# Kernel optimization log

Measured on AMD Instinct MI355X. Metric: run time of the kernel, lower is better.

## Reference

```python
import jax, jax.numpy as jnp
import numpy as np

STATE_SIZE, ACTION_SIZE, REWARD_SIZE = 128, 16, 4
IN = STATE_SIZE + REWARD_SIZE  # 132
B = 8192
W_NUM = 32


def _linear_params(key, fin, fout):
    k1, k2 = jax.random.split(key)
    s = 1.0 / np.sqrt(fin)
    w = jax.random.uniform(k1, (fout, fin), jnp.float32, -s, s)
    b = jax.random.uniform(k2, (fout,), jnp.float32, -s, s)
    return w, b


def setup_inputs() -> dict:
    key = jax.random.key(0)
    ks = jax.random.split(key, 7)
    w1, b1 = _linear_params(ks[0], IN, IN * 16)        # 132 -> 2112
    w2, b2 = _linear_params(ks[1], IN * 16, IN * 32)   # 2112 -> 4224
    w3, b3 = _linear_params(ks[2], IN * 32, IN * 64)   # 4224 -> 8448
    w4, b4 = _linear_params(ks[3], IN * 64, IN * 32)   # 8448 -> 4224
    wq, bq = _linear_params(ks[4], IN * 32, ACTION_SIZE * REWARD_SIZE)
    state = jax.random.normal(ks[5], (B, STATE_SIZE), jnp.float32)
    preference = jax.random.uniform(ks[6], (B, REWARD_SIZE), jnp.float32)
    return dict(state=state, preference=preference,
                w1=w1, b1=b1, w2=w2, b2=b2, w3=w3, b3=b3, w4=w4, b4=b4,
                wq=wq, bq=bq, w_num=W_NUM)


def _forward(state, preference, w1, b1, w2, b2, w3, b3, w4, b4, wq, bq, w_num):
    x = jnp.concatenate([state, preference], axis=1)              # [B, IN]
    h = jax.nn.relu(x @ w1.T + b1)
    h = jax.nn.relu(h @ w2.T + b2)
    h = jax.nn.relu(h @ w3.T + b3)
    h = jax.nn.relu(h @ w4.T + b4)
    q = (h @ wq.T + bq).reshape(-1, ACTION_SIZE, REWARD_SIZE)     # [B, A, R]

    s_num = preference.shape[0] // w_num
    # H(): envelope operator. The torch code repeat_interleaves flat_Q w_num
    # times per group; within each (w, s) group the preference vector is
    # constant, so inner products are constant across each run of w_num
    # repeated rows. argmax(dim=1)//w_num therefore equals argmax over the
    # action axis (first-tie semantics match). We compute that directly
    # without the O(w_num^2) blow-up -- identical math, identical output.
    qd = jax.lax.stop_gradient(q)                                 # Q.detach()
    rq = qd.reshape(s_num, w_num, ACTION_SIZE, REWARD_SIZE)
    rq = jnp.transpose(rq, (1, 0, 2, 3))                          # [w, s, A, R]
    rw = jnp.transpose(preference.reshape(s_num, w_num, REWARD_SIZE), (1, 0, 2))  # [w, s, R]
    ip = jnp.einsum('wsar,wsr->wsa', rq, rw)                      # [w, s, A]
    a_star = jnp.argmax(ip, axis=2)                               # [w, s]
    hq = jnp.take_along_axis(rq, a_star[..., None, None], axis=2)[:, :, 0, :]  # [w, s, R]
    hq = jnp.transpose(hq, (1, 0, 2)).reshape(-1, REWARD_SIZE)    # [s*w, R]
    return hq, q


def reference(state, preference, w1, b1, w2, b2, w3, b3, w4, b4, wq, bq, w_num):
    return _forward(state, preference, w1, b1, w2, b2, w3, b3, w4, b4, wq, bq, w_num)
```

## Files before the change

kernel.cpp:

```cpp
#include <hip/hip_runtime.h>


#define AS1 __attribute__((address_space(1)))
#define AS3 __attribute__((address_space(3)))

typedef _Float16 half8 __attribute__((ext_vector_type(8)));
typedef float floatx16 __attribute__((ext_vector_type(16)));

static constexpr float SCALE = 2048.0f;
static constexpr float INV_SCALE2 = 1.0f / (2048.0f * 2048.0f);

__global__ void split_w_kernel(const float* __restrict__ src, _Float16* __restrict__ hi,
                               _Float16* __restrict__ lo, int srcStride, int colOff,
                               int Kcopy, int Kpad) {
  int k = blockIdx.x * 256 + threadIdx.x;
  int n = blockIdx.y;
  if (k >= Kpad) return;
  float v = (k < Kcopy) ? src[(size_t)n * srcStride + colOff + k] * SCALE : 0.0f;
  _Float16 h = (_Float16)v;
  _Float16 l = (_Float16)(v - (float)h);
  size_t o = (size_t)n * Kpad + k;
  hi[o] = h;
  lo[o] = l;
}

__global__ void prep_x_kernel(const float* __restrict__ state, const float* __restrict__ pref,
                              _Float16* __restrict__ hi, _Float16* __restrict__ lo) {
  int k = threadIdx.x;
  int b = blockIdx.x;
  if (k >= 160) return;
  float v = 0.0f;
  if (k < 128) v = state[(size_t)b * 128 + k];
  else if (k < 132) v = pref[(size_t)b * 4 + (k - 128)];
  v *= SCALE;
  _Float16 h = (_Float16)v;
  _Float16 l = (_Float16)(v - (float)h);
  size_t o = (size_t)b * 160 + k;
  hi[o] = h;
  lo[o] = l;
}

__global__ __launch_bounds__(256) void gemm3_kernel(
    const _Float16* __restrict__ Ahi, const _Float16* __restrict__ Alo,
    const _Float16* __restrict__ Bhi, const _Float16* __restrict__ Blo,
    const float* __restrict__ bias,
    _Float16* __restrict__ Ohi, _Float16* __restrict__ Olo,
    float* __restrict__ Oacc,
    int K, int N, int mode, int accAdd) {
  __shared__ _Float16 lds[4 * 4096];
  const int tid = threadIdx.x;
  const int wave = tid >> 6;
  const int lane = tid & 63;
  const int m0 = blockIdx.x * 128;
  const int n0 = blockIdx.y * 128;

  const _Float16* gp[8];
  int loff[8];
#pragma unroll
  for (int j = 0; j < 8; ++j) {
    const int t = j >> 1;
    const int p = ((j & 1) << 8) + (wave << 6) + lane;
    const int r = p >> 2;
    const int g = (p & 3) ^ (r & 3);
    int row;
    const _Float16* plane;
    if (t < 2) {
      row = m0 + r;
      plane = t ? Alo : Ahi;
    } else {
      row = n0 + r;
      if (row > N - 1) row = N - 1;
      plane = (t == 3) ? Blo : Bhi;
    }
    gp[j] = plane + (size_t)row * K + 8 * g;
    loff[j] = t * 4096 + (((j & 1) << 8) + (wave << 6)) * 8;
  }

  const int wm = wave >> 1, wn = wave & 1;
  floatx16 acc[2][2];
#pragma unroll
  for (int i = 0; i < 2; ++i)
#pragma unroll
    for (int j = 0; j < 2; ++j)
#pragma unroll
      for (int e = 0; e < 16; ++e) acc[i][j][e] = 0.0f;

  const int rA0 = (wm << 6) + (lane & 31);
  const int rB0 = (wn << 6) + (lane & 31);
  const int gHalf = lane >> 5;

  const int nSteps = K >> 5;
  for (int ks = 0; ks < nSteps; ++ks) {
    __syncthreads();
#pragma unroll
    for (int j = 0; j < 8; ++j) {
      __builtin_amdgcn_global_load_lds((const AS1 unsigned int*)gp[j],
                                       (AS3 unsigned int*)&lds[loff[j]], 16, 0, 0);
      gp[j] += 32;
    }
    __syncthreads();
#pragma unroll
    for (int kh = 0; kh < 2; ++kh) {
      half8 ah[2], al[2], bh[2], bl[2];
#pragma unroll
      for (int i = 0; i < 2; ++i) {
        int rA = rA0 + (i << 5);
        int sA = (rA << 2) + (((kh << 1) + gHalf) ^ (rA & 3));
        ah[i] = *(const half8*)&lds[sA << 3];
        al[i] = *(const half8*)&lds[4096 + (sA << 3)];
        int rB = rB0 + (i << 5);
        int sB = (rB << 2) + (((kh << 1) + gHalf) ^ (rB & 3));
        bh[i] = *(const half8*)&lds[8192 + (sB << 3)];
        bl[i] = *(const half8*)&lds[12288 + (sB << 3)];
      }
#pragma unroll
      for (int i = 0; i < 2; ++i)
#pragma unroll
        for (int j = 0; j < 2; ++j) {
          acc[i][j] = __builtin_amdgcn_mfma_f32_32x32x16_f16(ah[i], bh[j], acc[i][j], 0, 0, 0);
          acc[i][j] = __builtin_amdgcn_mfma_f32_32x32x16_f16(ah[i], bl[j], acc[i][j], 0, 0, 0);
          acc[i][j] = __builtin_amdgcn_mfma_f32_32x32x16_f16(al[i], bh[j], acc[i][j], 0, 0, 0);
        }
    }
  }

#pragma unroll
  for (int i = 0; i < 2; ++i)
#pragma unroll
    for (int j = 0; j < 2; ++j)
#pragma unroll
      for (int e = 0; e < 16; ++e) {
        int row = m0 + (wm << 6) + (i << 5) + ((e & 3) + ((e >> 2) << 3) + ((lane >> 5) << 2));
        int col = n0 + (wn << 6) + (j << 5) + (lane & 31);
        if (col < N) {
          float v = acc[i][j][e] * INV_SCALE2;
          size_t o = (size_t)row * N + col;
          if (mode == 0) {
            v = fmaxf(v + bias[col], 0.0f) * SCALE;
            _Float16 h = (_Float16)v;
            _Float16 l = (_Float16)(v - (float)h);
            Ohi[o] = h;
            Olo[o] = l;
          } else {
            if (accAdd) v += Oacc[o];
            Oacc[o] = v;
          }
        }
      }
}

__global__ __launch_bounds__(256) void l5_finish_kernel(
    const float* __restrict__ acc4, const float* __restrict__ b4,
    const float* __restrict__ wq, const float* __restrict__ bq,
    const float* __restrict__ pref, float* __restrict__ out, int rowBase) {
  __shared__ __align__(16) float hbuf[4 * 4224];
  __shared__ float qbuf[4 * 64];
  __shared__ float ipbuf[4 * 16];
  const int t = threadIdx.x;
  const int r0 = blockIdx.x * 4;
#pragma unroll
  for (int r = 0; r < 4; ++r) {
    const float* src = acc4 + (size_t)(r0 + r) * 4224;
    for (int i = t; i < 4224; i += 256) hbuf[r * 4224 + i] = fmaxf(src[i] + b4[i], 0.0f);
  }
  __syncthreads();
  const int r = t >> 6, o = t & 63;
  const float* wrow = wq + (size_t)o * 4224;
  const float* hrow = &hbuf[r * 4224];
  float s = 0.0f;
  for (int k = 0; k < 4224; k += 4) {
    float4 h = *(const float4*)&hrow[k];
    float4 w = *(const float4*)&wrow[k];
    s += h.x * w.x + h.y * w.y + h.z * w.z + h.w * w.w;
  }
  s += bq[o];
  qbuf[r * 64 + o] = s;
  int grow = rowBase + r0 + r;
  out[32768 + (size_t)grow * 64 + o] = s;
  __syncthreads();
  if (t < 64) {
    int rr = t >> 4, a = t & 15;
    int g2 = rowBase + r0 + rr;
    float ip = 0.0f;
#pragma unroll
    for (int j = 0; j < 4; ++j) ip += qbuf[rr * 64 + a * 4 + j] * pref[(size_t)g2 * 4 + j];
    ipbuf[rr * 16 + a] = ip;
  }
  __syncthreads();
  if (t < 4) {
    int g2 = rowBase + r0 + t;
    float best = ipbuf[t * 16];
    int ba = 0;
#pragma unroll
    for (int a = 1; a < 16; ++a) {
      float v = ipbuf[t * 16 + a];
      if (v > best) { best = v; ba = a; }
    }
#pragma unroll
    for (int j = 0; j < 4; ++j) out[(size_t)g2 * 4 + j] = qbuf[t * 64 + ba * 4 + j];
  }
}

extern "C" void kernel_launch(void* const* d_in, const int* in_sizes, int n_in,
                              void* d_out, int out_size, void* d_ws, size_t ws_size,
                              hipStream_t stream) {
  const float* state = (const float*)d_in[0];
  const float* pref = (const float*)d_in[1];
  const float* w1 = (const float*)d_in[2];
  const float* b1 = (const float*)d_in[3];
  const float* w2 = (const float*)d_in[4];
  const float* b2 = (const float*)d_in[5];
  const float* w3 = (const float*)d_in[6];
  const float* b3 = (const float*)d_in[7];
  const float* w4 = (const float*)d_in[8];
  const float* b4 = (const float*)d_in[9];
  const float* wq = (const float*)d_in[10];
  const float* bq = (const float*)d_in[11];

  char* ws = (char*)d_ws;
  size_t off = 0;
  auto take = [&](size_t bytes) {
    size_t r = off;
    off += (bytes + 255) & ~(size_t)255;
    return r;
  };
  const size_t oW1h = take((size_t)2112 * 160 * 2);
  const size_t oW1l = take((size_t)2112 * 160 * 2);
  const size_t oW2h = take((size_t)4224 * 2112 * 2);
  const size_t oW2l = take((size_t)4224 * 2112 * 2);
  const size_t oW3h = take((size_t)2112 * 4224 * 2);
  const size_t oW3l = take((size_t)2112 * 4224 * 2);
  const size_t oW4h = take((size_t)4224 * 2112 * 2);
  const size_t oW4l = take((size_t)4224 * 2112 * 2);
  const size_t fixed = off;

  int Mc = 8192;
  while (Mc > 128 && fixed + (size_t)Mc * 51328 + 4096 > ws_size) Mc >>= 1;

  const size_t oXh = take((size_t)Mc * 160 * 2);
  const size_t oXl = take((size_t)Mc * 160 * 2);
  const size_t oH1h = take((size_t)Mc * 2112 * 2);
  const size_t oH1l = take((size_t)Mc * 2112 * 2);
  const size_t oH2h = take((size_t)Mc * 4224 * 2);
  const size_t oH2l = take((size_t)Mc * 4224 * 2);
  const size_t oH3h = take((size_t)Mc * 2112 * 2);
  const size_t oH3l = take((size_t)Mc * 2112 * 2);
  const size_t oACC = take((size_t)Mc * 4224 * 4);

  _Float16* W1h = (_Float16*)(ws + oW1h);
  _Float16* W1l = (_Float16*)(ws + oW1l);
  _Float16* W2h = (_Float16*)(ws + oW2h);
  _Float16* W2l = (_Float16*)(ws + oW2l);
  _Float16* W3h = (_Float16*)(ws + oW3h);
  _Float16* W3l = (_Float16*)(ws + oW3l);
  _Float16* W4h = (_Float16*)(ws + oW4h);
  _Float16* W4l = (_Float16*)(ws + oW4l);
  _Float16* Xh = (_Float16*)(ws + oXh);
  _Float16* Xl = (_Float16*)(ws + oXl);
  _Float16* H1h = (_Float16*)(ws + oH1h);
  _Float16* H1l = (_Float16*)(ws + oH1l);
  _Float16* H2h = (_Float16*)(ws + oH2h);
  _Float16* H2l = (_Float16*)(ws + oH2l);
  _Float16* H3h = (_Float16*)(ws + oH3h);
  _Float16* H3l = (_Float16*)(ws + oH3l);
  float* ACC = (float*)(ws + oACC);

  split_w_kernel<<<dim3(1, 2112), 256, 0, stream>>>(w1, W1h, W1l, 132, 0, 132, 160);
  split_w_kernel<<<dim3(9, 4224), 256, 0, stream>>>(w2, W2h, W2l, 2112, 0, 2112, 2112);

  const int NC = 8192 / Mc;
  const int GX = Mc / 128;
  for (int mc = 0; mc < NC; ++mc) {
    const float* st = state + (size_t)mc * Mc * 128;
    const float* pf = pref + (size_t)mc * Mc * 4;
    prep_x_kernel<<<dim3(Mc), 192, 0, stream>>>(st, pf, Xh, Xl);
    gemm3_kernel<<<dim3(GX, 17), 256, 0, stream>>>(Xh, Xl, W1h, W1l, b1, H1h, H1l,
                                                   nullptr, 160, 2112, 0, 0);
    gemm3_kernel<<<dim3(GX, 33), 256, 0, stream>>>(H1h, H1l, W2h, W2l, b2, H2h, H2l,
                                                   nullptr, 2112, 4224, 0, 0);
    for (int c = 0; c < 4; ++c) {
      split_w_kernel<<<dim3(17, 2112), 256, 0, stream>>>(w3 + (size_t)c * 2112 * 4224, W3h,
                                                         W3l, 4224, 0, 4224, 4224);
      split_w_kernel<<<dim3(9, 4224), 256, 0, stream>>>(w4, W4h, W4l, 8448, c * 2112, 2112,
                                                        2112);
      gemm3_kernel<<<dim3(GX, 17), 256, 0, stream>>>(H2h, H2l, W3h, W3l, b3 + c * 2112,
                                                     H3h, H3l, nullptr, 4224, 2112, 0, 0);
      gemm3_kernel<<<dim3(GX, 33), 256, 0, stream>>>(H3h, H3l, W4h, W4l, nullptr, nullptr,
                                                     nullptr, ACC, 2112, 4224, 1, c);
    }
    l5_finish_kernel<<<dim3(Mc / 4), 256, 0, stream>>>(ACC, b4, wq, bq, pref,
                                                       (float*)d_out, mc * Mc);
  }
}
```

Before: 6.243 ms.

## Run final Q layer on MFMA with split-K and fuse layer-4 bias/ReLU epilogue

Replaces the scalar fp32 l5_finish kernel with a split-fp16 MFMA GEMM over the last layer, using a new split-K grid dimension (4 slices) that writes partial sums which a light finish kernel reduces, biases and runs the envelope argmax on. The last layer-4 chunk now applies bias+ReLU and writes hi/lo fp16 activations directly, dropping the separate pass that re-read the fp32 accumulator. This removes a slow CUDA-core dot-product loop that read wq per row, at the cost of extra partial-sum traffic, a padded N=64 tile in a 128-wide kernel, and reuse of workspace buffers (H2, H1) as scratch.

```diff
diff --git a/kernel.cpp b/kernel.cpp
--- a/kernel.cpp
+++ b/kernel.cpp
@@ -46,13 +46,14 @@
     const float* __restrict__ bias,
     _Float16* __restrict__ Ohi, _Float16* __restrict__ Olo,
     float* __restrict__ Oacc,
-    int K, int N, int mode, int accAdd) {
+    int K, int N, int kPerZ, int mode, int accAdd, int Mrows) {
   __shared__ _Float16 lds[4 * 4096];
   const int tid = threadIdx.x;
   const int wave = tid >> 6;
   const int lane = tid & 63;
   const int m0 = blockIdx.x * 128;
   const int n0 = blockIdx.y * 128;
+  const int kBeg = blockIdx.z * kPerZ;
 
   const _Float16* gp[8];
   int loff[8];
@@ -72,7 +73,7 @@
       if (row > N - 1) row = N - 1;
       plane = (t == 3) ? Blo : Bhi;
     }
-    gp[j] = plane + (size_t)row * K + 8 * g;
+    gp[j] = plane + (size_t)row * K + kBeg + 8 * g;
     loff[j] = t * 4096 + (((j & 1) << 8) + (wave << 6)) * 8;
   }
 
@@ -89,7 +90,7 @@
   const int rB0 = (wn << 6) + (lane & 31);
   const int gHalf = lane >> 5;
 
-  const int nSteps = K >> 5;
+  const int nSteps = kPerZ >> 5;
   for (int ks = 0; ks < nSteps; ++ks) {
     __syncthreads();
 #pragma unroll
@@ -134,71 +135,64 @@
         int col = n0 + (wn << 6) + (j << 5) + (lane & 31);
         if (col < N) {
           float v = acc[i][j][e] * INV_SCALE2;
-          size_t o = (size_t)row * N + col;
           if (mode == 0) {
+            size_t o = (size_t)row * N + col;
             v = fmaxf(v + bias[col], 0.0f) * SCALE;
             _Float16 h = (_Float16)v;
             _Float16 l = (_Float16)(v - (float)h);
             Ohi[o] = h;
             Olo[o] = l;
-          } else {
+          } else if (mode == 1) {
+            size_t o = ((size_t)blockIdx.z * Mrows + row) * N + col;
             if (accAdd) v += Oacc[o];
             Oacc[o] = v;
+          } else {
+            size_t o = (size_t)row * N + col;
+            v += Oacc[o];
+            v = fmaxf(v + bias[col], 0.0f) * SCALE;
+            _Float16 h = (_Float16)v;
+            _Float16 l = (_Float16)(v - (float)h);
+            Ohi[o] = h;
+            Olo[o] = l;
           }
         }
       }
 }
 
-__global__ __launch_bounds__(256) void l5_finish_kernel(
-    const float* __restrict__ acc4, const float* __restrict__ b4,
-    const float* __restrict__ wq, const float* __restrict__ bq,
-    const float* __restrict__ pref, float* __restrict__ out, int rowBase) {
-  __shared__ __align__(16) float hbuf[4 * 4224];
-  __shared__ float qbuf[4 * 64];
-  __shared__ float ipbuf[4 * 16];
-  const int t = threadIdx.x;
-  const int r0 = blockIdx.x * 4;
-#pragma unroll
-  for (int r = 0; r < 4; ++r) {
-    const float* src = acc4 + (size_t)(r0 + r) * 4224;
-    for (int i = t; i < 4224; i += 256) hbuf[r * 4224 + i] = fmaxf(src[i] + b4[i], 0.0f);
-  }
-  __syncthreads();
-  const int r = t >> 6, o = t & 63;
-  const float* wrow = wq + (size_t)o * 4224;
-  const float* hrow = &hbuf[r * 4224];
-  float s = 0.0f;
-  for (int k = 0; k < 4224; k += 4) {
-    float4 h = *(const float4*)&hrow[k];
-    float4 w = *(const float4*)&wrow[k];
-    s += h.x * w.x + h.y * w.y + h.z * w.z + h.w * w.w;
-  }
-  s += bq[o];
-  qbuf[r * 64 + o] = s;
-  int grow = rowBase + r0 + r;
-  out[32768 + (size_t)grow * 64 + o] = s;
-  __syncthreads();
-  if (t < 64) {
-    int rr = t >> 4, a = t & 15;
-    int g2 = rowBase + r0 + rr;
-    float ip = 0.0f;
-#pragma unroll
-    for (int j = 0; j < 4; ++j) ip += qbuf[rr * 64 + a * 4 + j] * pref[(size_t)g2 * 4 + j];
-    ipbuf[rr * 16 + a] = ip;
-  }
-  __syncthreads();
-  if (t < 4) {
-    int g2 = rowBase + r0 + t;
-    float best = ipbuf[t * 16];
-    int ba = 0;
-#pragma unroll
-    for (int a = 1; a < 16; ++a) {
-      float v = ipbuf[t * 16 + a];
-      if (v > best) { best = v; ba = a; }
-    }
-#pragma unroll
-    for (int j = 0; j < 4; ++j) out[(size_t)g2 * 4 + j] = qbuf[t * 64 + ba * 4 + j];
-  }
+__global__ __launch_bounds__(128) void finish_kernel(
+    const float* __restrict__ part, const float* __restrict__ bq,
+    const float* __restrict__ pref, float* __restrict__ out, int rowBase, int Mc) {
+  int b = blockIdx.x * 128 + threadIdx.x;
+  if (b >= Mc) return;
+  float q[64];
+#pragma unroll
+  for (int o4 = 0; o4 < 16; ++o4) {
+    float4 s = *(const float4*)&part[(size_t)b * 64 + o4 * 4];
+    float4 s1 = *(const float4*)&part[(size_t)(Mc + b) * 64 + o4 * 4];
+    float4 s2 = *(const float4*)&part[(size_t)(2 * Mc + b) * 64 + o4 * 4];
+    float4 s3 = *(const float4*)&part[(size_t)(3 * Mc + b) * 64 + o4 * 4];
+    float4 bb = *(const float4*)&bq[o4 * 4];
+    q[o4 * 4 + 0] = s.x + s1.x + s2.x + s3.x + bb.x;
+    q[o4 * 4 + 1] = s.y + s1.y + s2.y + s3.y + bb.y;
+    q[o4 * 4 + 2] = s.z + s1.z + s2.z + s3.z + bb.z;
+    q[o4 * 4 + 3] = s.w + s1.w + s2.w + s3.w + bb.w;
+  }
+  int g = rowBase + b;
+  float* qout = out + 32768 + (size_t)g * 64;
+#pragma unroll
+  for (int o4 = 0; o4 < 16; ++o4)
+    *(float4*)&qout[o4 * 4] = make_float4(q[o4 * 4], q[o4 * 4 + 1], q[o4 * 4 + 2], q[o4 * 4 + 3]);
+  float p0 = pref[(size_t)g * 4 + 0], p1 = pref[(size_t)g * 4 + 1];
+  float p2 = pref[(size_t)g * 4 + 2], p3 = pref[(size_t)g * 4 + 3];
+  float best = q[0] * p0 + q[1] * p1 + q[2] * p2 + q[3] * p3;
+  int ba = 0;
+#pragma unroll
+  for (int a = 1; a < 16; ++a) {
+    float ip = q[4 * a] * p0 + q[4 * a + 1] * p1 + q[4 * a + 2] * p2 + q[4 * a + 3] * p3;
+    if (ip > best) { best = ip; ba = a; }
+  }
+  *(float4*)&out[(size_t)g * 4] =
+      make_float4(q[4 * ba], q[4 * ba + 1], q[4 * ba + 2], q[4 * ba + 3]);
 }
 
 extern "C" void kernel_launch(void* const* d_in, const int* in_sizes, int n_in,
@@ -232,6 +226,8 @@
   const size_t oW3l = take((size_t)2112 * 4224 * 2);
   const size_t oW4h = take((size_t)4224 * 2112 * 2);
   const size_t oW4l = take((size_t)4224 * 2112 * 2);
+  const size_t oW5h = take((size_t)64 * 4224 * 2);
+  const size_t oW5l = take((size_t)64 * 4224 * 2);
   const size_t fixed = off;
 
   int Mc = 8192;
@@ -255,6 +251,8 @@
   _Float16* W3l = (_Float16*)(ws + oW3l);
   _Float16* W4h = (_Float16*)(ws + oW4h);
   _Float16* W4l = (_Float16*)(ws + oW4l);
+  _Float16* W5h = (_Float16*)(ws + oW5h);
+  _Float16* W5l = (_Float16*)(ws + oW5l);
   _Float16* Xh = (_Float16*)(ws + oXh);
   _Float16* Xl = (_Float16*)(ws + oXl);
   _Float16* H1h = (_Float16*)(ws + oH1h);
@@ -264,9 +262,13 @@
   _Float16* H3h = (_Float16*)(ws + oH3h);
   _Float16* H3l = (_Float16*)(ws + oH3l);
   float* ACC = (float*)(ws + oACC);
+  _Float16* H4h = H2h;
+  _Float16* H4l = H2l;
+  float* QP = (float*)(ws + oH1h);
 
   split_w_kernel<<<dim3(1, 2112), 256, 0, stream>>>(w1, W1h, W1l, 132, 0, 132, 160);
   split_w_kernel<<<dim3(9, 4224), 256, 0, stream>>>(w2, W2h, W2l, 2112, 0, 2112, 2112);
+  split_w_kernel<<<dim3(17, 64), 256, 0, stream>>>(wq, W5h, W5l, 4224, 0, 4224, 4224);
 
   const int NC = 8192 / Mc;
   const int GX = Mc / 128;
@@ -275,20 +277,29 @@
     const float* pf = pref + (size_t)mc * Mc * 4;
     prep_x_kernel<<<dim3(Mc), 192, 0, stream>>>(st, pf, Xh, Xl);
     gemm3_kernel<<<dim3(GX, 17), 256, 0, stream>>>(Xh, Xl, W1h, W1l, b1, H1h, H1l,
-                                                   nullptr, 160, 2112, 0, 0);
+                                                   nullptr, 160, 2112, 160, 0, 0, Mc);
     gemm3_kernel<<<dim3(GX, 33), 256, 0, stream>>>(H1h, H1l, W2h, W2l, b2, H2h, H2l,
-                                                   nullptr, 2112, 4224, 0, 0);
+                                                   nullptr, 2112, 4224, 2112, 0, 0, Mc);
     for (int c = 0; c < 4; ++c) {
       split_w_kernel<<<dim3(17, 2112), 256, 0, stream>>>(w3 + (size_t)c * 2112 * 4224, W3h,
                                                          W3l, 4224, 0, 4224, 4224);
       split_w_kernel<<<dim3(9, 4224), 256, 0, stream>>>(w4, W4h, W4l, 8448, c * 2112, 2112,
                                                         2112);
       gemm3_kernel<<<dim3(GX, 17), 256, 0, stream>>>(H2h, H2l, W3h, W3l, b3 + c * 2112,
-                                                     H3h, H3l, nullptr, 4224, 2112, 0, 0);
-      gemm3_kernel<<<dim3(GX, 33), 256, 0, stream>>>(H3h, H3l, W4h, W4l, nullptr, nullptr,
-                                                     nullptr, ACC, 2112, 4224, 1, c);
+                                                     H3h, H3l, nullptr, 4224, 2112, 4224,
+                                                     0, 0, Mc);
+      if (c < 3) {
+        gemm3_kernel<<<dim3(GX, 33), 256, 0, stream>>>(H3h, H3l, W4h, W4l, nullptr, nullptr,
+                                                       nullptr, ACC, 2112, 4224, 2112, 1,
+                                                       c > 0 ? 1 : 0, Mc);
+      } else {
+        gemm3_kernel<<<dim3(GX, 33), 256, 0, stream>>>(H3h, H3l, W4h, W4l, b4, H4h, H4l,
+                                                       ACC, 2112, 4224, 2112, 2, 0, Mc);
+      }
     }
-    l5_finish_kernel<<<dim3(Mc / 4), 256, 0, stream>>>(ACC, b4, wq, bq, pref,
-                                                       (float*)d_out, mc * Mc);
-  }
-}
+    gemm3_kernel<<<dim3(GX, 1, 4), 256, 0, stream>>>(H4h, H4l, W5h, W5l, nullptr, nullptr,
+                                                     nullptr, QP, 4224, 64, 1056, 1, 0, Mc);
+    finish_kernel<<<dim3(Mc / 128), 128, 0, stream>>>(QP, bq, pref, (float*)d_out,
+                                                      mc * Mc, Mc);
+  }
+}
```

Result: faster. 5.397 ms (-13.6%).
